# Kernel optimization log

Measured on AMD Instinct MI355X. Metric: run time of the kernel, lower is better.

The kernel has to match this reference:

```python
import jax, jax.numpy as jnp
import numpy as np

B, P, NOBJ, C = 32, 16384, 50, 21
THRESHOLD, NEG_POS_RATIO, ALPHA = 0.5, 3.0, 1.0


def cxcy_to_xy(c):
    return jnp.concatenate([c[:, :2] - c[:, 2:] / 2, c[:, :2] + c[:, 2:] / 2], axis=1)


def xy_to_cxcy(xy):
    return jnp.concatenate([(xy[:, :2] + xy[:, 2:]) / 2, xy[:, 2:] - xy[:, :2]], axis=1)


def cxcy_to_gcxgcy(cxcy, priors_cxcy):
    # standard SSD encoding with variances 0.1 / 0.2
    g_cxcy = (cxcy[:, :2] - priors_cxcy[:, :2]) / (priors_cxcy[:, 2:] / 10.0)
    g_wh = jnp.log(cxcy[:, 2:] / priors_cxcy[:, 2:]) * 5.0
    return jnp.concatenate([g_cxcy, g_wh], axis=1)


def jaccard(a, b):
    # a: [N,4] xyxy, b: [P,4] xyxy -> [N,P]
    lt = jnp.maximum(a[:, None, :2], b[None, :, :2])
    rb = jnp.minimum(a[:, None, 2:], b[None, :, 2:])
    inter = jnp.clip(rb - lt, 0.0).prod(-1)
    area_a = (a[:, 2:] - a[:, :2]).prod(-1)
    area_b = (b[:, 2:] - b[:, :2]).prod(-1)
    return inter / (area_a[:, None] + area_b[None, :] - inter)


def setup_inputs() -> dict:
    key = jax.random.key(0)
    k1, k2, k3, k4, k5, k6, k7 = jax.random.split(key, 7)
    predicted_locs = jax.random.normal(k1, (B, P, 4), dtype=jnp.float32)
    predicted_scores = jax.random.normal(k2, (B, P, C), dtype=jnp.float32)
    # ground-truth boxes: valid xyxy in [0,1] with positive extent
    ccx = jax.random.uniform(k3, (B, NOBJ, 2), minval=0.1, maxval=0.9)
    wh = jax.random.uniform(k4, (B, NOBJ, 2), minval=0.02, maxval=0.2)
    boxes = jnp.concatenate([ccx - wh / 2, ccx + wh / 2], axis=-1).astype(jnp.float32)
    labels = jax.random.randint(k5, (B, NOBJ), 1, C)  # object labels are >= 1 (0 = background)
    pcxy = jax.random.uniform(k6, (P, 2), minval=0.05, maxval=0.95)
    pwh = jax.random.uniform(k7, (P, 2), minval=0.02, maxval=0.4)
    priors_cxcy = jnp.concatenate([pcxy, pwh], axis=-1).astype(jnp.float32)
    return dict(predicted_locs=predicted_locs, predicted_scores=predicted_scores,
                boxes=boxes, labels=labels, priors_cxcy=priors_cxcy)


def reference(predicted_locs, predicted_scores, boxes, labels, priors_cxcy):
    priors_xy = cxcy_to_xy(priors_cxcy)

    def assign(boxes_i, labels_i):
        ov = jaccard(boxes_i, priors_xy)                    # [N,P]
        overlap_for_prior = ov.max(axis=0)                  # [P]
        object_for_prior = ov.argmax(axis=0)                # [P]
        prior_for_object = ov.argmax(axis=1)                # [N]
        # force each object to own its best prior
        object_for_prior = object_for_prior.at[prior_for_object].set(jnp.arange(NOBJ))
        overlap_for_prior = overlap_for_prior.at[prior_for_object].set(1.0)
        label_for_prior = labels_i[object_for_prior]
        label_for_prior = jnp.where(overlap_for_prior < THRESHOLD, 0, label_for_prior)
        assigned_xy = boxes_i[object_for_prior]             # [P,4]
        true_locs_i = cxcy_to_gcxgcy(xy_to_cxcy(assigned_xy), priors_cxcy)
        return true_locs_i, label_for_prior

    true_locs, true_classes = jax.vmap(assign)(boxes, labels)  # [B,P,4], [B,P]

    pos = true_classes != 0                                 # [B,P]
    n_pos = pos.sum(axis=1)                                 # [B]
    n_pos_total = n_pos.sum().astype(jnp.float32)

    # nn.L1Loss(): mean abs error over positive prior entries (Npos*4 elements)
    l1 = jnp.abs(predicted_locs - true_locs) * pos[..., None]
    loc_loss = l1.sum() / (n_pos_total * 4.0)

    # per-prior cross entropy
    logp = jax.nn.log_softmax(predicted_scores, axis=-1)    # [B,P,C]
    ce = -jnp.take_along_axis(logp, true_classes[..., None], axis=-1)[..., 0]  # [B,P]

    conf_pos = jnp.where(pos, ce, 0.0).sum()
    neg = jnp.where(pos, 0.0, ce)
    neg_sorted = -jnp.sort(-neg, axis=1)                    # descending per image
    ranks = jnp.arange(P)[None, :].astype(jnp.float32)
    hard = ranks < (NEG_POS_RATIO * n_pos.astype(jnp.float32))[:, None]
    conf_hard_neg = jnp.where(hard, neg_sorted, 0.0).sum()

    conf_loss = (conf_hard_neg + conf_pos) / n_pos_total
    return conf_loss + ALPHA * loc_loss
```

## Files before the change

kernel.cpp:

```cpp
#include <hip/hip_runtime.h>
#include <hip/hip_bf16.h>
#include <float.h>

#define BB   32
#define PP   16384
#define NOBJ 50
#define NCLS 21
#define PBLK 64
#define NBLK (BB * PBLK)
#define NGRP 7
#define NCHK 8
#define CPRI 2048
#define JPT  8


__global__ __launch_bounds__(256) void k_iou(
    const float* __restrict__ boxes, const float* __restrict__ priors,
    unsigned long long* __restrict__ bp_part,
    unsigned long long* __restrict__ ovp_part)
{
#pragma clang fp contract(off)
    const int blk   = (int)blockIdx.x;
    const int b     = blk / (NGRP * NCHK);
    const int rem   = blk % (NGRP * NCHK);
    const int g     = rem / NCHK;
    const int c     = rem % NCHK;
    const int n0    = g * 8;
    const int pbase = c * CPRI;
    const int t     = (int)threadIdx.x;

    __shared__ unsigned long long sbest[8];
    if (t < 8) sbest[t] = 0ull;

    float ax0[8], ay0[8], ax1[8], ay1[8], aarea[8];
#pragma unroll
    for (int k = 0; k < 8; ++k) {
        int nn = n0 + k; if (nn >= NOBJ) nn = NOBJ - 1;
        float4 bx = reinterpret_cast<const float4*>(boxes)[b * NOBJ + nn];
        ax0[k] = bx.x; ay0[k] = bx.y; ax1[k] = bx.z; ay1[k] = bx.w;
        aarea[k] = (bx.z - bx.x) * (bx.w - bx.y);
    }

    float px0[JPT], py0[JPT], px1[JPT], py1[JPT], pab[JPT];
#pragma unroll
    for (int j = 0; j < JPT; ++j) {
        float4 pc = reinterpret_cast<const float4*>(priors)[pbase + t + j * 256];
        float hx = pc.z * 0.5f, hy = pc.w * 0.5f;
        px0[j] = pc.x - hx; py0[j] = pc.y - hy;
        px1[j] = pc.x + hx; py1[j] = pc.y + hy;
        pab[j] = (px1[j] - px0[j]) * (py1[j] - py0[j]);
    }

    float bof[8];  int bop[8];
    float bpf[JPT]; int bpn[JPT];
#pragma unroll
    for (int k = 0; k < 8; ++k) { bof[k] = -1.0f; bop[k] = 0; }
#pragma unroll
    for (int j = 0; j < JPT; ++j) { bpf[j] = -1.0f; bpn[j] = 0; }

#pragma unroll
    for (int k = 0; k < 8; ++k) {
#pragma unroll
        for (int j = 0; j < JPT; ++j) {
            float ltx = fmaxf(ax0[k], px0[j]), lty = fmaxf(ay0[k], py0[j]);
            float rbx = fminf(ax1[k], px1[j]), rby = fminf(ay1[k], py1[j]);
            float dx = fmaxf(rbx - ltx, 0.0f);
            float dy = fmaxf(rby - lty, 0.0f);
            float inter = dx * dy;
            float iou = __fdividef(inter, (aarea[k] + pab[j]) - inter);
            if (iou > bof[k]) { bof[k] = iou; bop[k] = pbase + t + j * 256; }
            if (iou > bpf[j]) { bpf[j] = iou; bpn[j] = n0 + k; }
        }
    }

#pragma unroll
    for (int j = 0; j < JPT; ++j) {
        unsigned long long key =
            ((unsigned long long)__float_as_uint(bpf[j]) << 32) |
            (unsigned long long)(unsigned)(NOBJ - 1 - bpn[j]);
        ovp_part[((size_t)g * BB + b) * PP + pbase + t + j * 256] = key;
    }

    __syncthreads();
#pragma unroll
    for (int k = 0; k < 8; ++k) {
        unsigned long long v =
            ((unsigned long long)__float_as_uint(bof[k]) << 32) |
            (unsigned long long)(0xFFFFFFFFu - (unsigned)bop[k]);
        for (int o = 32; o > 0; o >>= 1) {
            unsigned long long other = __shfl_down(v, o, 64);
            if (other > v) v = other;
        }
        if ((t & 63) == 0) atomicMax(&sbest[k], v);
    }
    __syncthreads();
    if (t < 8 && n0 + t < NOBJ)
        bp_part[(size_t)c * BB * NOBJ + b * NOBJ + n0 + t] = sbest[t];
}

__global__ __launch_bounds__(256) void k_main(
    const float* __restrict__ locs, const float* __restrict__ scores,
    const float* __restrict__ boxes, const int* __restrict__ labels,
    const float* __restrict__ priors,
    const unsigned long long* __restrict__ bp_part,
    const unsigned long long* __restrict__ ovp_part,
    float* __restrict__ neg, double* __restrict__ pc_conf,
    double* __restrict__ pc_loc, int* __restrict__ pc_npos)
{
#pragma clang fp contract(off)
    const int b   = (int)blockIdx.x >> 6;
    const int p0  = ((int)blockIdx.x & 63) << 8;
    const int t   = (int)threadIdx.x;
    const int p   = p0 + t;
    const int idx = b * PP + p;

    __shared__ float  sls[256 * NCLS];
    __shared__ int    sforce[256];
    __shared__ float4 sbox[NOBJ];
    __shared__ int    slab[NOBJ];
    __shared__ double sconf[4], sloc[4];
    __shared__ int    snp[4];

    {
        const float4* gsc = reinterpret_cast<const float4*>(
            scores + (size_t)(b * PP + p0) * NCLS);
        float4* dls = reinterpret_cast<float4*>(sls);
#pragma unroll
        for (int i = 0; i < 6; ++i) {
            int j = i * 256 + t;
            if (j < (256 * NCLS) / 4) dls[j] = gsc[j];
        }
    }
    sforce[t] = -1;
    if (t < NOBJ) {
        sbox[t] = reinterpret_cast<const float4*>(boxes)[b * NOBJ + t];
        slab[t] = labels[b * NOBJ + t];
    }
    __syncthreads();
    if (t < NOBJ) {
        unsigned long long k0 = bp_part[b * NOBJ + t];
#pragma unroll
        for (int cc = 1; cc < NCHK; ++cc) {
            unsigned long long kc = bp_part[(size_t)cc * BB * NOBJ + b * NOBJ + t];
            if (kc > k0) k0 = kc;
        }
        int spf = (int)(0xFFFFFFFFu - (unsigned)(k0 & 0xFFFFFFFFull));
        if (spf >= p0 && spf < p0 + 256)
            atomicMax(&sforce[spf - p0], t);
    }
    __syncthreads();

    unsigned long long key = ovp_part[(size_t)b * PP + p];
#pragma unroll
    for (int g = 1; g < NGRP; ++g) {
        unsigned long long kg = ovp_part[((size_t)g * BB + b) * PP + p];
        if (kg > key) key = kg;
    }
    int   bestn = NOBJ - 1 - (int)((unsigned)key & 63u);
    float v     = __uint_as_float((unsigned)(key >> 32));
    int fn = sforce[t];
    if (fn >= 0) { bestn = fn; v = 1.0f; }

    int lbl = slab[bestn];
    if (v < 0.5f) lbl = 0;
    const bool pos = (lbl != 0);

    float locl1 = 0.0f;
    if (pos) {
        float4 bx = sbox[bestn];
        float4 pc = reinterpret_cast<const float4*>(priors)[p];
        float cx = (bx.x + bx.z) / 2.0f;
        float cy = (bx.y + bx.w) / 2.0f;
        float w  = bx.z - bx.x, h = bx.w - bx.y;
        float gx = (cx - pc.x) / (pc.z / 10.0f);
        float gy = (cy - pc.y) / (pc.w / 10.0f);
        float gw = logf(w / pc.z) * 5.0f;
        float gh = logf(h / pc.w) * 5.0f;
        float4 pl = reinterpret_cast<const float4*>(locs)[idx];
        locl1 = fabsf(pl.x - gx) + fabsf(pl.y - gy) +
                fabsf(pl.z - gw) + fabsf(pl.w - gh);
    }

    float x[NCLS];
    float m = -FLT_MAX;
#pragma unroll
    for (int c = 0; c < NCLS; ++c) { x[c] = sls[t * NCLS + c]; m = fmaxf(m, x[c]); }
    float tgt = sls[t * NCLS + lbl];
    float s = 0.0f;
#pragma unroll
    for (int c = 0; c < NCLS; ++c) s += expf(x[c] - m);
    float ce = (logf(s) + m) - tgt;

    neg[idx] = pos ? 0.0f : ce;

    float cp = pos ? ce : 0.0f;
    unsigned long long bal = __ballot(pos);
    float s1 = cp, s2 = locl1;
    for (int o = 32; o > 0; o >>= 1) {
        s1 += __shfl_down(s1, o, 64);
        s2 += __shfl_down(s2, o, 64);
    }
    if ((t & 63) == 0) {
        int w = t >> 6;
        sconf[w] = (double)s1;
        sloc[w]  = (double)s2;
        snp[w]   = (int)__popcll(bal);
    }
    __syncthreads();
    if (t == 0) {
        pc_conf[blockIdx.x] = sconf[0] + sconf[1] + sconf[2] + sconf[3];
        pc_loc[blockIdx.x]  = sloc[0] + sloc[1] + sloc[2] + sloc[3];
        pc_npos[blockIdx.x] = snp[0] + snp[1] + snp[2] + snp[3];
    }
}

__global__ __launch_bounds__(1024) void k_topk(
    const float* __restrict__ neg, const int* __restrict__ pc_npos,
    double* __restrict__ hard)
{
    const int b    = (int)blockIdx.x;
    const int t    = (int)threadIdx.x;
    const int lane = t & 63;
    const int wid  = t >> 6;

    __shared__ unsigned hist[64 * 257];
    __shared__ unsigned ssuf[256];
    __shared__ unsigned s_bb, s_above;
    __shared__ float swave[16];
    __shared__ int s_np;

    if (t < 64) {
        int v = pc_npos[b * PBLK + t];
        for (int o = 32; o > 0; o >>= 1) v += __shfl_down(v, o, 64);
        if (t == 0) s_np = v;
    }

    float v[16];
    {
        const float4* g = reinterpret_cast<const float4*>(neg + (size_t)b * PP);
#pragma unroll
        for (int i = 0; i < 4; ++i) {
            float4 q = g[i * 1024 + t];
            v[i*4+0] = q.x; v[i*4+1] = q.y; v[i*4+2] = q.z; v[i*4+3] = q.w;
        }
    }
    __syncthreads();

    long long K = 3LL * (long long)s_np;
    if (K > PP) K = PP;
    unsigned remaining = (unsigned)K;
    unsigned prefix = 0, mask = 0;
    float mySum = 0.0f;

    for (int shift = 24; shift >= 0; shift -= 8) {
        for (int i = t; i < 64 * 257; i += 1024) hist[i] = 0;
        __syncthreads();
        unsigned* h = hist + lane * 257;
#pragma unroll
        for (int i = 0; i < 16; ++i) {
            unsigned u = __float_as_uint(v[i]);
            if ((u & mask) == prefix) atomicAdd(&h[(u >> shift) & 255u], 1u);
        }
        __syncthreads();
        unsigned cnt = 0;
        if (t < 256) {
#pragma unroll
            for (int w = 0; w < 64; ++w) cnt += hist[w * 257 + t];
            ssuf[t] = cnt;
        }
        __syncthreads();
        for (int off = 1; off < 256; off <<= 1) {
            unsigned add = 0;
            if (t < 256 && t + off < 256) add = ssuf[t + off];
            __syncthreads();
            if (t < 256) ssuf[t] += add;
            __syncthreads();
        }
        if (t < 256) {
            unsigned suf = ssuf[t];
            if (suf >= remaining && suf - cnt < remaining) {
                s_bb = (unsigned)t; s_above = suf - cnt;
            }
        }
        __syncthreads();
        unsigned bb = s_bb;
#pragma unroll
        for (int i = 0; i < 16; ++i) {
            unsigned u = __float_as_uint(v[i]);
            if ((u & mask) == prefix && ((u >> shift) & 255u) > bb)
                mySum += v[i];
        }
        remaining -= s_above;
        prefix |= bb << shift;
        mask   |= 255u << shift;
        __syncthreads();
    }

    float s = mySum;
    for (int o = 32; o > 0; o >>= 1) s += __shfl_down(s, o, 64);
    if ((t & 63) == 0) swave[wid] = s;
    __syncthreads();
    if (t == 0) {
        float tot = 0.0f;
        for (int w = 0; w < 16; ++w) tot += swave[w];
        if (remaining) tot += (float)remaining * __uint_as_float(prefix);
        hard[b] = (double)tot;
    }
}

__global__ __launch_bounds__(256) void k_final(
    const double* __restrict__ pc_conf, const double* __restrict__ pc_loc,
    const int* __restrict__ pc_npos, const double* __restrict__ hard,
    float* __restrict__ out)
{
    const int t = (int)threadIdx.x;
    __shared__ double sa[4], sb[4], sh[4];
    __shared__ int sn[4];
    double a = 0.0, c = 0.0, h = 0.0; int np = 0;
    for (int i = t; i < NBLK; i += 256) {
        a += pc_conf[i]; c += pc_loc[i]; np += pc_npos[i];
    }
    if (t < BB) h = hard[t];
    for (int o = 32; o > 0; o >>= 1) {
        a += __shfl_down(a, o, 64);
        c += __shfl_down(c, o, 64);
        h += __shfl_down(h, o, 64);
        np += __shfl_down(np, o, 64);
    }
    if ((t & 63) == 0) { int w = t >> 6; sa[w]=a; sb[w]=c; sh[w]=h; sn[w]=np; }
    __syncthreads();
    if (t == 0) {
        double at = sa[0]+sa[1]+sa[2]+sa[3];
        double ct = sb[0]+sb[1]+sb[2]+sb[3];
        double ht = sh[0]+sh[1]+sh[2]+sh[3];
        double npt = (double)(sn[0]+sn[1]+sn[2]+sn[3]);
        out[0] = (float)((at + ht) / npt + ct / (npt * 4.0));
    }
}

extern "C" void kernel_launch(void* const* d_in, const int* in_sizes, int n_in,
                              void* d_out, int out_size, void* d_ws, size_t ws_size,
                              hipStream_t stream) {
    const float* locs   = (const float*)d_in[0];
    const float* scores = (const float*)d_in[1];
    const float* boxes  = (const float*)d_in[2];
    const int*   labels = (const int*)d_in[3];
    const float* priors = (const float*)d_in[4];

    char* ws = (char*)d_ws;
    unsigned long long* bp_part = (unsigned long long*)ws;
    double* pc_conf = (double*)(ws + 262144);
    double* pc_loc  = (double*)(ws + 278528);
    int*    pc_npos = (int*)(ws + 294912);
    double* hard    = (double*)(ws + 303104);
    unsigned long long* ovp_part = (unsigned long long*)(ws + 327680);
    float*  neg     = (float*)(ws + 33554432);
    float*  out     = (float*)d_out;

    hipLaunchKernelGGL(k_iou,   dim3(BB * NGRP * NCHK), dim3(256),  0, stream,
                       boxes, priors, bp_part, ovp_part);
    hipLaunchKernelGGL(k_main,  dim3(NBLK),             dim3(256),  0, stream,
                       locs, scores, boxes, labels, priors, bp_part, ovp_part,
                       neg, pc_conf, pc_loc, pc_npos);
    hipLaunchKernelGGL(k_topk,  dim3(BB),               dim3(1024), 0, stream,
                       neg, pc_npos, hard);
    hipLaunchKernelGGL(k_final, dim3(1),                dim3(256),  0, stream,
                       pc_conf, pc_loc, pc_npos, hard, out);
}
```

Baseline: 75.18 us.

## Split IoU into per-prior and per-object kernels to drop partial-result traffic

The combined IoU kernel wrote 7 partial per-prior keys per (image, prior), which the main kernel then reduced. It is replaced by two kernels. k_prior loops over all 50 objects per prior and writes one final key. k_obj computes each object's best prior over two halves of the prior set, with one wave per object. This cuts global write and read traffic for the partials, roughly 29 MB down to 4 MB, at the cost of computing every IoU twice and adding an extra kernel launch.

Result: slower. 88.68 us (+18.0%).

```diff
diff --git a/kernel.cpp b/kernel.cpp
--- a/kernel.cpp
+++ b/kernel.cpp
@@ -8,94 +8,101 @@
 #define NCLS 21
 #define PBLK 64
 #define NBLK (BB * PBLK)
-#define NGRP 7
-#define NCHK 8
-#define CPRI 2048
-#define JPT  8
-
-
-__global__ __launch_bounds__(256) void k_iou(
+#define OGRP 13
+
+
+__global__ __launch_bounds__(256) void k_prior(
     const float* __restrict__ boxes, const float* __restrict__ priors,
-    unsigned long long* __restrict__ bp_part,
-    unsigned long long* __restrict__ ovp_part)
+    unsigned long long* __restrict__ perprior)
 {
 #pragma clang fp contract(off)
-    const int blk   = (int)blockIdx.x;
-    const int b     = blk / (NGRP * NCHK);
-    const int rem   = blk % (NGRP * NCHK);
-    const int g     = rem / NCHK;
-    const int c     = rem % NCHK;
-    const int n0    = g * 8;
-    const int pbase = c * CPRI;
+    const int b     = (int)blockIdx.x >> 5;
+    const int pbase = ((int)blockIdx.x & 31) << 9;
     const int t     = (int)threadIdx.x;
 
-    __shared__ unsigned long long sbest[8];
-    if (t < 8) sbest[t] = 0ull;
-
-    float ax0[8], ay0[8], ax1[8], ay1[8], aarea[8];
-#pragma unroll
-    for (int k = 0; k < 8; ++k) {
-        int nn = n0 + k; if (nn >= NOBJ) nn = NOBJ - 1;
-        float4 bx = reinterpret_cast<const float4*>(boxes)[b * NOBJ + nn];
-        ax0[k] = bx.x; ay0[k] = bx.y; ax1[k] = bx.z; ay1[k] = bx.w;
-        aarea[k] = (bx.z - bx.x) * (bx.w - bx.y);
-    }
-
-    float px0[JPT], py0[JPT], px1[JPT], py1[JPT], pab[JPT];
-#pragma unroll
-    for (int j = 0; j < JPT; ++j) {
+    __shared__ float4 sbox[NOBJ];
+    if (t < NOBJ) sbox[t] = reinterpret_cast<const float4*>(boxes)[b * NOBJ + t];
+
+    float px0[2], py0[2], px1[2], py1[2], pab[2];
+#pragma unroll
+    for (int j = 0; j < 2; ++j) {
         float4 pc = reinterpret_cast<const float4*>(priors)[pbase + t + j * 256];
         float hx = pc.z * 0.5f, hy = pc.w * 0.5f;
         px0[j] = pc.x - hx; py0[j] = pc.y - hy;
         px1[j] = pc.x + hx; py1[j] = pc.y + hy;
         pab[j] = (px1[j] - px0[j]) * (py1[j] - py0[j]);
     }
-
-    float bof[8];  int bop[8];
-    float bpf[JPT]; int bpn[JPT];
-#pragma unroll
-    for (int k = 0; k < 8; ++k) { bof[k] = -1.0f; bop[k] = 0; }
-#pragma unroll
-    for (int j = 0; j < JPT; ++j) { bpf[j] = -1.0f; bpn[j] = 0; }
-
-#pragma unroll
-    for (int k = 0; k < 8; ++k) {
-#pragma unroll
-        for (int j = 0; j < JPT; ++j) {
-            float ltx = fmaxf(ax0[k], px0[j]), lty = fmaxf(ay0[k], py0[j]);
-            float rbx = fminf(ax1[k], px1[j]), rby = fminf(ay1[k], py1[j]);
+    __syncthreads();
+
+    float bf[2] = {-1.0f, -1.0f}; int bn[2] = {0, 0};
+#pragma unroll 10
+    for (int n = 0; n < NOBJ; ++n) {
+        float4 bx = sbox[n];
+        float aarea = (bx.z - bx.x) * (bx.w - bx.y);
+#pragma unroll
+        for (int j = 0; j < 2; ++j) {
+            float ltx = fmaxf(bx.x, px0[j]), lty = fmaxf(bx.y, py0[j]);
+            float rbx = fminf(bx.z, px1[j]), rby = fminf(bx.w, py1[j]);
             float dx = fmaxf(rbx - ltx, 0.0f);
             float dy = fmaxf(rby - lty, 0.0f);
             float inter = dx * dy;
-            float iou = __fdividef(inter, (aarea[k] + pab[j]) - inter);
-            if (iou > bof[k]) { bof[k] = iou; bop[k] = pbase + t + j * 256; }
-            if (iou > bpf[j]) { bpf[j] = iou; bpn[j] = n0 + k; }
-        }
-    }
-
-#pragma unroll
-    for (int j = 0; j < JPT; ++j) {
+            float iou = __fdividef(inter, (aarea + pab[j]) - inter);
+            if (iou > bf[j]) { bf[j] = iou; bn[j] = n; }
+        }
+    }
+#pragma unroll
+    for (int j = 0; j < 2; ++j) {
         unsigned long long key =
-            ((unsigned long long)__float_as_uint(bpf[j]) << 32) |
-            (unsigned long long)(unsigned)(NOBJ - 1 - bpn[j]);
-        ovp_part[((size_t)g * BB + b) * PP + pbase + t + j * 256] = key;
-    }
-
-    __syncthreads();
-#pragma unroll
-    for (int k = 0; k < 8; ++k) {
-        unsigned long long v =
-            ((unsigned long long)__float_as_uint(bof[k]) << 32) |
-            (unsigned long long)(0xFFFFFFFFu - (unsigned)bop[k]);
-        for (int o = 32; o > 0; o >>= 1) {
-            unsigned long long other = __shfl_down(v, o, 64);
-            if (other > v) v = other;
-        }
-        if ((t & 63) == 0) atomicMax(&sbest[k], v);
-    }
-    __syncthreads();
-    if (t < 8 && n0 + t < NOBJ)
-        bp_part[(size_t)c * BB * NOBJ + b * NOBJ + n0 + t] = sbest[t];
+            ((unsigned long long)__float_as_uint(bf[j]) << 32) |
+            (unsigned long long)(unsigned)(NOBJ - 1 - bn[j]);
+        perprior[(size_t)b * PP + pbase + t + j * 256] = key;
+    }
+}
+
+__global__ __launch_bounds__(256) void k_obj(
+    const float* __restrict__ boxes, const float* __restrict__ priors,
+    unsigned long long* __restrict__ bp_part)
+{
+#pragma clang fp contract(off)
+    const int blk = (int)blockIdx.x;
+    const int b   = blk / (OGRP * 2);
+    const int rem = blk % (OGRP * 2);
+    const int og  = rem >> 1;
+    const int h   = rem & 1;
+    const int t   = (int)threadIdx.x;
+    const int w   = t >> 6, l = t & 63;
+
+    const int n  = og * 4 + w;
+    const int nn = n < NOBJ ? n : NOBJ - 1;
+    float4 bx = reinterpret_cast<const float4*>(boxes)[b * NOBJ + nn];
+    float aarea = (bx.z - bx.x) * (bx.w - bx.y);
+
+    const float4* gpri = reinterpret_cast<const float4*>(priors) + h * 8192;
+    float bf = -1.0f; int bp = 0;
+#pragma unroll 8
+    for (int i = 0; i < 128; ++i) {
+        float4 pc = gpri[i * 64 + l];
+        float hx = pc.z * 0.5f, hy = pc.w * 0.5f;
+        float px0 = pc.x - hx, py0 = pc.y - hy;
+        float px1 = pc.x + hx, py1 = pc.y + hy;
+        float pab = (px1 - px0) * (py1 - py0);
+        float ltx = fmaxf(bx.x, px0), lty = fmaxf(bx.y, py0);
+        float rbx = fminf(bx.z, px1), rby = fminf(bx.w, py1);
+        float dx = fmaxf(rbx - ltx, 0.0f);
+        float dy = fmaxf(rby - lty, 0.0f);
+        float inter = dx * dy;
+        float iou = __fdividef(inter, (aarea + pab) - inter);
+        if (iou > bf) { bf = iou; bp = h * 8192 + i * 64 + l; }
+    }
+    unsigned long long v =
+        ((unsigned long long)__float_as_uint(bf) << 32) |
+        (unsigned long long)(0xFFFFFFFFu - (unsigned)bp);
+    for (int o = 32; o > 0; o >>= 1) {
+        unsigned long long other = __shfl_down(v, o, 64);
+        if (other > v) v = other;
+    }
+    if (l == 0 && n < NOBJ)
+        bp_part[(size_t)h * BB * 64 + b * 64 + n] = v;
 }
 
 __global__ __launch_bounds__(256) void k_main(
@@ -103,7 +110,7 @@
     const float* __restrict__ boxes, const int* __restrict__ labels,
     const float* __restrict__ priors,
     const unsigned long long* __restrict__ bp_part,
-    const unsigned long long* __restrict__ ovp_part,
+    const unsigned long long* __restrict__ perprior,
     float* __restrict__ neg, double* __restrict__ pc_conf,
     double* __restrict__ pc_loc, int* __restrict__ pc_npos)
 {
@@ -138,24 +145,16 @@
     }
     __syncthreads();
     if (t < NOBJ) {
-        unsigned long long k0 = bp_part[b * NOBJ + t];
-#pragma unroll
-        for (int cc = 1; cc < NCHK; ++cc) {
-            unsigned long long kc = bp_part[(size_t)cc * BB * NOBJ + b * NOBJ + t];
-            if (kc > k0) k0 = kc;
-        }
+        unsigned long long k0 = bp_part[b * 64 + t];
+        unsigned long long k1 = bp_part[(size_t)BB * 64 + b * 64 + t];
+        if (k1 > k0) k0 = k1;
         int spf = (int)(0xFFFFFFFFu - (unsigned)(k0 & 0xFFFFFFFFull));
         if (spf >= p0 && spf < p0 + 256)
             atomicMax(&sforce[spf - p0], t);
     }
     __syncthreads();
 
-    unsigned long long key = ovp_part[(size_t)b * PP + p];
-#pragma unroll
-    for (int g = 1; g < NGRP; ++g) {
-        unsigned long long kg = ovp_part[((size_t)g * BB + b) * PP + p];
-        if (kg > key) key = kg;
-    }
+    unsigned long long key = perprior[(size_t)b * PP + p];
     int   bestn = NOBJ - 1 - (int)((unsigned)key & 63u);
     float v     = __uint_as_float((unsigned)(key >> 32));
     int fn = sforce[t];
@@ -353,17 +352,19 @@
     double* pc_loc  = (double*)(ws + 278528);
     int*    pc_npos = (int*)(ws + 294912);
     double* hard    = (double*)(ws + 303104);
-    unsigned long long* ovp_part = (unsigned long long*)(ws + 327680);
+    unsigned long long* perprior = (unsigned long long*)(ws + 327680);
     float*  neg     = (float*)(ws + 33554432);
     float*  out     = (float*)d_out;
 
-    hipLaunchKernelGGL(k_iou,   dim3(BB * NGRP * NCHK), dim3(256),  0, stream,
-                       boxes, priors, bp_part, ovp_part);
-    hipLaunchKernelGGL(k_main,  dim3(NBLK),             dim3(256),  0, stream,
-                       locs, scores, boxes, labels, priors, bp_part, ovp_part,
+    hipLaunchKernelGGL(k_prior, dim3(BB * 32),       dim3(256),  0, stream,
+                       boxes, priors, perprior);
+    hipLaunchKernelGGL(k_obj,   dim3(BB * OGRP * 2), dim3(256),  0, stream,
+                       boxes, priors, bp_part);
+    hipLaunchKernelGGL(k_main,  dim3(NBLK),          dim3(256),  0, stream,
+                       locs, scores, boxes, labels, priors, bp_part, perprior,
                        neg, pc_conf, pc_loc, pc_npos);
-    hipLaunchKernelGGL(k_topk,  dim3(BB),               dim3(1024), 0, stream,
+    hipLaunchKernelGGL(k_topk,  dim3(BB),            dim3(1024), 0, stream,
                        neg, pc_npos, hard);
-    hipLaunchKernelGGL(k_final, dim3(1),                dim3(256),  0, stream,
+    hipLaunchKernelGGL(k_final, dim3(1),             dim3(256),  0, stream,
                        pc_conf, pc_loc, pc_npos, hard, out);
 }
```
